# Optimization experiments

Hardware: AMD Instinct MI355X
Metric: run time of the kernel (lower is better)

## Reference

```python
import jax, jax.numpy as jnp
import numpy as np

N, IN_DIM, HEADS, C = 100000, 128, 4, 32  # out_dim = HEADS*C = 128
E = 1600000


def setup_inputs() -> dict:
    key = jax.random.key(0)
    ks = jax.random.split(key, 9)
    x = jax.random.normal(ks[0], (N, IN_DIM), dtype=jnp.float32)
    edge_index = jax.random.randint(ks[1], (2, E), 0, N, dtype=jnp.int64)
    # GATConv params
    W = jax.random.normal(ks[2], (HEADS * C, IN_DIM), dtype=jnp.float32) * (1.0 / np.sqrt(IN_DIM))
    att_src = jax.random.normal(ks[3], (HEADS, C), dtype=jnp.float32) * 0.1
    att_dst = jax.random.normal(ks[4], (HEADS, C), dtype=jnp.float32) * 0.1
    bias = jax.random.normal(ks[5], (HEADS * C,), dtype=jnp.float32) * 0.01
    # complex phase + LayerNorm params
    phase = jax.random.normal(ks[6], (HEADS * C,), dtype=jnp.float32) * 0.02
    gamma = 1.0 + jax.random.normal(ks[7], (HEADS * C,), dtype=jnp.float32) * 0.01
    beta = jax.random.normal(ks[8], (HEADS * C,), dtype=jnp.float32) * 0.01
    return {"x": x, "edge_index": edge_index, "W": W, "att_src": att_src,
            "att_dst": att_dst, "bias": bias, "phase": phase, "gamma": gamma, "beta": beta}


def reference(x, edge_index, W, att_src, att_dst, bias, phase, gamma, beta):
    src, dst = edge_index[0], edge_index[1]
    h = (x @ W.T).reshape(N, HEADS, C)                      # [N,H,C]
    a_src = jnp.einsum('nhc,hc->nh', h, att_src)            # [N,H]
    a_dst = jnp.einsum('nhc,hc->nh', h, att_dst)
    e = jax.nn.leaky_relu(a_src[src] + a_dst[dst], 0.2)     # [E,H]
    # segment softmax over destination nodes (numerically stable)
    m = jax.ops.segment_max(e, dst, num_segments=N)         # [N,H]
    ex = jnp.exp(e - m[dst])
    s = jax.ops.segment_sum(ex, dst, num_segments=N)        # [N,H]
    alpha = ex / (s[dst] + 1e-16)                           # [E,H]
    msg = h[src] * alpha[:, :, None]                        # [E,H,C]
    out = jax.ops.segment_sum(msg, dst, num_segments=N).reshape(N, HEADS * C) + bias
    # complex phase magnitude: sqrt((h cos p)^2 + (h sin p)^2 + eps)
    mag = jnp.sqrt((out * jnp.cos(phase)) ** 2 + (out * jnp.sin(phase)) ** 2 + 1e-12)
    # LayerNorm
    mu = mag.mean(-1, keepdims=True)
    var = ((mag - mu) ** 2).mean(-1, keepdims=True)
    hn = (mag - mu) / jnp.sqrt(var + 1e-5) * gamma + beta
    return jax.nn.gelu(hn, approximate=False)
```

## Files before the change

kernel.cpp:

```cpp
#include <hip/hip_runtime.h>
#include <hip/hip_bf16.h>

#define N_ 100000
#define E_ 1600000
#define D_ 128
#define H_ 4
#define C_ 32
#define XSTR 136

using bf16 = __hip_bfloat16;
typedef __attribute__((ext_vector_type(8))) short short8;
typedef __attribute__((ext_vector_type(4))) float f32x4;

__device__ __forceinline__ float u2f(unsigned u) { return __uint_as_float(u); }
__device__ __forceinline__ unsigned short f2bu(float v) {
  bf16 t = __float2bfloat16(v);
  return *(unsigned short*)&t;
}

__global__ __launch_bounds__(256) void k_linear_link(
    const float* __restrict__ x, const float* __restrict__ W,
    const float* __restrict__ att_src, const float* __restrict__ att_dst,
    const int* __restrict__ ei, int* __restrict__ head4,
    int2* __restrict__ nxt2, bf16* __restrict__ h,
    float* __restrict__ a_src, float* __restrict__ a_dst) {
  __shared__ unsigned short WB[16384];
  __shared__ unsigned short XS[64 * XSTR];
  __shared__ float ats[128], atd[128];
  const int tid = threadIdx.x;

  for (int e = blockIdx.x * 256 + tid; e < E_; e += gridDim.x * 256) {
    const int d = ei[E_ + e];
    const int prev = atomicExch(&head4[d * 4 + (e & 3)], e);
    nxt2[e] = make_int2(ei[e], prev);
  }

  const int lane = tid & 63, w = tid >> 6;
  const int n15 = lane & 15, quad = lane >> 4;

  for (int i = tid; i < 16384; i += 256) {
    const int n = i >> 7, k = i & 127;
    const int kk = k >> 5, q = (k >> 3) & 3, j = k & 7;
    const int frag = kk * 8 + (n >> 4);
    WB[frag * 512 + q * 128 + (n & 15) * 8 + j] = f2bu(W[n * 128 + k]);
  }
  if (tid < 128) { ats[tid] = att_src[tid]; atd[tid] = att_dst[tid]; }

  const int nrb = (N_ + 63) / 64;
  for (int rb = blockIdx.x; rb < nrb; rb += gridDim.x) {
    const int row0 = rb * 64;
    __syncthreads();
    for (int idx = tid; idx < 2048; idx += 256) {
      const int r = idx >> 5;
      const int c = (idx & 31) * 4;
      float4 xv = make_float4(0.f, 0.f, 0.f, 0.f);
      if (row0 + r < N_) xv = *(const float4*)&x[(size_t)(row0 + r) * 128 + c];
      ushort4 o;
      o.x = f2bu(xv.x); o.y = f2bu(xv.y); o.z = f2bu(xv.z); o.w = f2bu(xv.w);
      *(ushort4*)&XS[r * XSTR + c] = o;
    }
    __syncthreads();

    f32x4 acc[8] = {};
    const int arow = w * 16 + n15;
#pragma unroll
    for (int kk = 0; kk < 4; kk++) {
      const short8 a = *(const short8*)&XS[arow * XSTR + kk * 32 + quad * 8];
#pragma unroll
      for (int t = 0; t < 8; t++) {
        const short8 b = *(const short8*)&WB[(kk * 8 + t) * 512 + lane * 8];
        acc[t] = __builtin_amdgcn_mfma_f32_16x16x32_bf16(a, b, acc[t], 0, 0, 0);
      }
    }

    __syncthreads();
#pragma unroll
    for (int t = 0; t < 8; t++)
#pragma unroll
      for (int reg = 0; reg < 4; reg++)
        XS[(w * 16 + quad * 4 + reg) * XSTR + t * 16 + n15] =
            f2bu(acc[t][reg]);
    __syncthreads();
    {
      const int row = tid >> 2;
      const int hd = tid & 3;
      const int cb = hd * 32;
      const int grow = row0 + row;
      float ps = 0.f, pd = 0.f;
      if (grow < N_) {
#pragma unroll
        for (int g = 0; g < 4; g++) {
          const uint4 v = *(const uint4*)&XS[row * XSTR + cb + g * 8];
          *(uint4*)&h[(size_t)grow * 128 + cb + g * 8] = v;
          const unsigned uu[4] = {v.x, v.y, v.z, v.w};
#pragma unroll
          for (int p = 0; p < 4; p++) {
            const float f0 = u2f(uu[p] << 16);
            const float f1 = u2f(uu[p] & 0xffff0000u);
            const int cc = cb + g * 8 + p * 2;
            ps = fmaf(f0, ats[cc], ps);     ps = fmaf(f1, ats[cc + 1], ps);
            pd = fmaf(f0, atd[cc], pd);     pd = fmaf(f1, atd[cc + 1], pd);
          }
        }
        a_src[grow * 4 + hd] = ps;
        a_dst[grow * 4 + hd] = pd;
      }
    }
  }
}

__global__ __launch_bounds__(256) void k_gather4(
    const int* __restrict__ head4, const int2* __restrict__ nxt2,
    const float* __restrict__ a_src, const float* __restrict__ a_dst,
    const bf16* __restrict__ h, const float* __restrict__ bias,
    const float* __restrict__ gamma, const float* __restrict__ beta,
    float* __restrict__ out) {
  const int lane = threadIdx.x & 63;
  const int d = blockIdx.x * 4 + (threadIdx.x >> 6);
  if (d >= N_) return;
  const int head = lane >> 4;
  const int srcsel = lane & 48;
  const float ad = a_dst[d * 4 + head];
  const int ch = lane * 2;

  int e = head4[d * 4 + (lane & 3)];
  float acc0 = 0.f, acc1 = 0.f, sumw_mine = 0.f;

  while (__any(e != -1)) {
    const int c = (e < 0) ? 0 : e;
    const int2 sn = nxt2[c];
    const int s = sn.x;
    float ev = a_src[s * 4 + head] + ad;
    ev = (ev > 0.f) ? ev : 0.2f * ev;
    const float w = (e < 0) ? 0.f : __expf(ev);
    sumw_mine += w;
    const int soff = s << 7;

#pragma unroll
    for (int j = 0; j < 4; j++) {
      const float wj = __shfl(w, srcsel | j);
      const int oj = __shfl(soff, j);
      const __hip_bfloat162 hv = *(const __hip_bfloat162*)&h[oj + ch];
      acc0 = fmaf(wj, __low2float(hv), acc0);
      acc1 = fmaf(wj, __high2float(hv), acc1);
    }
    e = (e < 0) ? -1 : sn.y;
  }

  float sumw = sumw_mine;
  sumw += __shfl_xor(sumw, 1);
  sumw += __shfl_xor(sumw, 2);

  const float inv = 1.0f / (sumw + 1e-16f);
  const float2 bi = *(const float2*)&bias[ch];
  const float v0 = acc0 * inv + bi.x;
  const float v1 = acc1 * inv + bi.y;
  const float m0i = sqrtf(v0 * v0 + 1e-12f);
  const float m1i = sqrtf(v1 * v1 + 1e-12f);

  float s1 = m0i + m1i;
#pragma unroll
  for (int off = 32; off > 0; off >>= 1) s1 += __shfl_xor(s1, off);
  const float mu = s1 * (1.0f / 128.0f);
  const float d0 = m0i - mu, d1 = m1i - mu;
  float q = d0 * d0 + d1 * d1;
#pragma unroll
  for (int off = 32; off > 0; off >>= 1) q += __shfl_xor(q, off);
  const float rstd = rsqrtf(q * (1.0f / 128.0f) + 1e-5f);
  const float2 ga = *(const float2*)&gamma[ch];
  const float2 be = *(const float2*)&beta[ch];
  const float hn0 = d0 * rstd * ga.x + be.x;
  const float hn1 = d1 * rstd * ga.y + be.y;
  const float g0 = 0.5f * hn0 * (1.0f + erff(hn0 * 0.70710678118654752f));
  const float g1 = 0.5f * hn1 * (1.0f + erff(hn1 * 0.70710678118654752f));
  *(float2*)&out[(size_t)d * 128 + ch] = make_float2(g0, g1);
}

extern "C" void kernel_launch(void* const* d_in, const int* in_sizes, int n_in,
                              void* d_out, int out_size, void* d_ws, size_t ws_size,
                              hipStream_t stream) {
  const float* x       = (const float*)d_in[0];
  const int*   ei      = (const int*)d_in[1];
  const float* W       = (const float*)d_in[2];
  const float* att_src = (const float*)d_in[3];
  const float* att_dst = (const float*)d_in[4];
  const float* bias    = (const float*)d_in[5];
  const float* gamma   = (const float*)d_in[7];
  const float* beta    = (const float*)d_in[8];
  float* out = (float*)d_out;

  bf16*  h     = (bf16*)d_ws;
  float* a_src = (float*)(h + (size_t)N_ * D_);
  float* a_dst = a_src + (size_t)N_ * H_;
  int*   head4 = (int*)(a_dst + (size_t)N_ * H_);
  int2*  nxt2  = (int2*)(head4 + (size_t)N_ * 4);

  hipMemsetAsync(head4, 0xFF, (size_t)N_ * 4 * sizeof(int), stream);

  k_linear_link<<<768, 256, 0, stream>>>(x, W, att_src, att_dst, ei, head4,
                                         nxt2, h, a_src, a_dst);
  k_gather4<<<(N_ + 3) / 4, 256, 0, stream>>>(head4, nxt2, a_src, a_dst, h,
                                              bias, gamma, beta, out);
}
```

Measured before the change: 333.7 us.

## Split each destination's four edge chains across two wavefronts with prefetch

Each destination node is now handled by two wavefronts, each walking two of the four linked-list chains. Partial sums are combined through shared memory, and the second wavefront exits after a block barrier. The next list node is also prefetched before the current edge is processed, which shortens the dependent pointer-chasing latency per iteration. In exchange, the grid launches twice as many wavefronts, adds a shared-memory reduction and barrier, and half the waves sit idle during the normalization epilogue.

```diff
diff --git a/kernel.cpp b/kernel.cpp
--- a/kernel.cpp
+++ b/kernel.cpp
@@ -115,41 +115,57 @@
     const bf16* __restrict__ h, const float* __restrict__ bias,
     const float* __restrict__ gamma, const float* __restrict__ beta,
     float* __restrict__ out) {
-  const int lane = threadIdx.x & 63;
-  const int d = blockIdx.x * 4 + (threadIdx.x >> 6);
-  if (d >= N_) return;
+  const int tid = threadIdx.x;
+  const int lane = tid & 63;
+  const int wsub = (tid >> 6) & 1;
+  const int slot = tid >> 7;
+  const int d = blockIdx.x * 2 + slot;
   const int head = lane >> 4;
   const int srcsel = lane & 48;
   const float ad = a_dst[d * 4 + head];
   const int ch = lane * 2;
 
-  int e = head4[d * 4 + (lane & 3)];
+  __shared__ float accsh[2][128];
+  __shared__ float sumsh[2][4];
+
+  int e = head4[d * 4 + (lane & 1) + wsub * 2];
+  int2 sn = nxt2[(e < 0) ? 0 : e];
   float acc0 = 0.f, acc1 = 0.f, sumw_mine = 0.f;
 
   while (__any(e != -1)) {
-    const int c = (e < 0) ? 0 : e;
-    const int2 sn = nxt2[c];
+    const int enext = (e < 0) ? -1 : sn.y;
+    const int2 sn_pf = nxt2[(enext < 0) ? 0 : enext];
     const int s = sn.x;
     float ev = a_src[s * 4 + head] + ad;
     ev = (ev > 0.f) ? ev : 0.2f * ev;
     const float w = (e < 0) ? 0.f : __expf(ev);
     sumw_mine += w;
     const int soff = s << 7;
-
-#pragma unroll
-    for (int j = 0; j < 4; j++) {
+#pragma unroll
+    for (int j = 0; j < 2; j++) {
       const float wj = __shfl(w, srcsel | j);
       const int oj = __shfl(soff, j);
       const __hip_bfloat162 hv = *(const __hip_bfloat162*)&h[oj + ch];
       acc0 = fmaf(wj, __low2float(hv), acc0);
       acc1 = fmaf(wj, __high2float(hv), acc1);
     }
-    e = (e < 0) ? -1 : sn.y;
-  }
-
-  float sumw = sumw_mine;
-  sumw += __shfl_xor(sumw, 1);
-  sumw += __shfl_xor(sumw, 2);
+    e = enext;
+    sn = sn_pf;
+  }
+
+  sumw_mine += __shfl_xor(sumw_mine, 1);
+
+  if (wsub == 1) {
+    accsh[slot][ch] = acc0;
+    accsh[slot][ch + 1] = acc1;
+    sumsh[slot][head] = sumw_mine;
+  }
+  __syncthreads();
+  if (wsub == 1) return;
+
+  acc0 += accsh[slot][ch];
+  acc1 += accsh[slot][ch + 1];
+  const float sumw = sumw_mine + sumsh[slot][head];
 
   const float inv = 1.0f / (sumw + 1e-16f);
   const float2 bi = *(const float2*)&bias[ch];
@@ -199,6 +215,6 @@
 
   k_linear_link<<<768, 256, 0, stream>>>(x, W, att_src, att_dst, ei, head4,
                                          nxt2, h, a_src, a_dst);
-  k_gather4<<<(N_ + 3) / 4, 256, 0, stream>>>(head4, nxt2, a_src, a_dst, h,
-                                              bias, gamma, beta, out);
-}
+  k_gather4<<<N_ / 2, 256, 0, stream>>>(head4, nxt2, a_src, a_dst, h,
+                                        bias, gamma, beta, out);
+}
```

Result: slower. 385.3 us (+15.4%).
